# Optimization experiments

Hardware: AMD Instinct MI355X
Metric: run time of the kernel (lower is better)

Reference implementation:

```python
import jax, jax.numpy as jnp
import numpy as np

F4_MAX = 6.0      # float4 e2m1 max magnitude
F8_MAX = 448.0    # float8 e4m3 max magnitude
BLOCK = 16        # nvfp4 block size along reduction dim


def _fp4_e2m1_rne(v):
    """Round v to the nearest float4 e2m1 value, ties-to-even.
    Representable magnitudes: {0, 0.5, 1, 1.5, 2, 3, 4, 6}."""
    s = jnp.sign(v)
    a = jnp.clip(jnp.abs(v), 0.0, F4_MAX)
    # exponent of the quantization step: subnormals and [1,2) share step 0.5
    e = jnp.clip(jnp.floor(jnp.log2(jnp.maximum(a, 1.0))), 0.0, 2.0)
    step = jnp.exp2(e - 1.0)  # 0.5, 1.0 or 2.0
    q = jnp.round(a / step) * step  # jnp.round is round-half-to-even
    return s * jnp.clip(q, 0.0, F4_MAX)


def _nvfp4_quant_dequant(x, global_scale):
    """scaled_fp4_quant followed by dequant (== what the scaled fp4 GEMM
    with alpha = 1/(gs_a*gs_w) computes per operand)."""
    lead, K = x.shape[:-1], x.shape[-1]
    xb = x.reshape(*lead, K // BLOCK, BLOCK)
    amax = jnp.max(jnp.abs(xb), axis=-1, keepdims=True)            # per-block amax
    scale = (amax * (global_scale / F4_MAX))
    scale = scale.astype(jnp.float8_e4m3fn).astype(jnp.float32)    # e4m3 block scale
    safe = jnp.where(scale > 0.0, scale, 1.0)
    q = _fp4_e2m1_rne(xb * (global_scale / safe))                  # fp4 codes (as floats)
    dq = q * safe / global_scale                                   # dequantized values
    return dq.reshape(x.shape)


def setup_inputs() -> dict:
    key = jax.random.key(0)
    k1, k2, k3 = jax.random.split(key, 3)
    B, S, K, N = 4, 2048, 4096, 4096
    x = jax.random.normal(k1, (B, S, K), dtype=jnp.float32)
    W = jax.random.normal(k2, (N, K), dtype=jnp.float32) * 0.02
    bias = jax.random.normal(k3, (N,), dtype=jnp.float32) * 0.02
    return {"x": x, "W": W, "bias": bias}


def reference(x, W, bias):
    # per-tensor global scales (FLOAT8_E4M3_MAX * FLOAT4_E2M1_MAX / amax)
    x_gs = (F8_MAX * F4_MAX) / jnp.max(jnp.abs(x)).astype(jnp.float32)
    w_gs = (F8_MAX * F4_MAX) / jnp.max(jnp.abs(W)).astype(jnp.float32)
    x_dq = _nvfp4_quant_dequant(x, x_gs)   # [B,S,K]
    w_dq = _nvfp4_quant_dequant(W, w_gs)   # [N,K]
    out = jnp.einsum('bsk,nk->bsn', x_dq, w_dq) + bias
    return out.astype(x.dtype)
```

## Files before the change

kernel.cpp:

```cpp
#include <hip/hip_runtime.h>
#include <stdint.h>

typedef unsigned short u16;
typedef __bf16 bf16x8 __attribute__((ext_vector_type(8)));
typedef float floatx4 __attribute__((ext_vector_type(4)));

__global__ void amax_both_k(const float4* __restrict__ x, long nx4,
                            const float4* __restrict__ w, long nw4,
                            unsigned* slots, int gx) {
    const float4* src; long n4; int bid, nb; unsigned* slot;
    if ((int)blockIdx.x < gx) { src = x; n4 = nx4; bid = blockIdx.x; nb = gx; slot = slots; }
    else { src = w; n4 = nw4; bid = blockIdx.x - gx; nb = gridDim.x - gx; slot = slots + 1; }
    float m = 0.0f;
    long stride = (long)nb * blockDim.x;
    for (long i = (long)bid * blockDim.x + threadIdx.x; i < n4; i += stride) {
        float4 v = src[i];
        m = fmaxf(m, fmaxf(fmaxf(fabsf(v.x), fabsf(v.y)), fmaxf(fabsf(v.z), fabsf(v.w))));
    }
    #pragma unroll
    for (int off = 32; off > 0; off >>= 1)
        m = fmaxf(m, __shfl_down(m, off, 64));
    __shared__ float sm[4];
    int lane = threadIdx.x & 63, wv = threadIdx.x >> 6;
    if (lane == 0) sm[wv] = m;
    __syncthreads();
    if (threadIdx.x == 0) {
        m = fmaxf(fmaxf(sm[0], sm[1]), fmaxf(sm[2], sm[3]));
        atomicMax(slot, __float_as_uint(m));
    }
}

__device__ __forceinline__ float e4m3_rne(float v) {
    unsigned u = __float_as_uint(v);
    u += 0x7FFFFu + ((u >> 20) & 1u);
    float hi = __uint_as_float(u & 0xFFF00000u);
    float lo = rintf(v * 512.0f) * 0.001953125f;
    return (v < 0.015625f) ? lo : hi;
}

__device__ __forceinline__ float fp4_rne(float x) {
    float a = fminf(fabsf(x), 6.0f);
    unsigned u = __float_as_uint(a);
    u += 0x1FFFFFu + ((u >> 22) & 1u);
    float hi = __uint_as_float(u & 0xFFC00000u);
    float lo = rintf(a + a) * 0.5f;
    float q = (a < 1.0f) ? lo : hi;
    return copysignf(q, x);
}

__device__ __forceinline__ unsigned pack2(float d0, float d1) {
    return (__float_as_uint(d0) >> 16) | (__float_as_uint(d1) & 0xFFFF0000u);
}

__global__ void quant_both_k(const float* __restrict__ x, const float* __restrict__ W,
                             u16* __restrict__ Aq, u16* __restrict__ Bq,
                             const unsigned* __restrict__ slots, long nbx, long nbtot) {
    long b = (long)blockIdx.x * blockDim.x + threadIdx.x;
    if (b >= nbtot) return;
    const float* src; u16* dst; float ag;
    if (b < nbx) { src = x + b * 16; dst = Aq + b * 16; ag = __uint_as_float(slots[0]); }
    else { long c = b - nbx; src = W + c * 16; dst = Bq + c * 16; ag = __uint_as_float(slots[1]); }
    float gs = 2688.0f / ag;
    float t  = gs / 6.0f;
    const float4* p = (const float4*)src;
    float4 v0 = p[0], v1 = p[1], v2 = p[2], v3 = p[3];
    float am = 0.0f;
    am = fmaxf(am, fmaxf(fmaxf(fabsf(v0.x), fabsf(v0.y)), fmaxf(fabsf(v0.z), fabsf(v0.w))));
    am = fmaxf(am, fmaxf(fmaxf(fabsf(v1.x), fabsf(v1.y)), fmaxf(fabsf(v1.z), fabsf(v1.w))));
    am = fmaxf(am, fmaxf(fmaxf(fabsf(v2.x), fabsf(v2.y)), fmaxf(fabsf(v2.z), fabsf(v2.w))));
    am = fmaxf(am, fmaxf(fmaxf(fabsf(v3.x), fabsf(v3.y)), fmaxf(fabsf(v3.z), fabsf(v3.w))));
    float sf = e4m3_rne(am * t);
    float r = gs / (sf > 0.0f ? sf : 1.0f);
    uint4 o0, o1;
    o0.x = pack2(fp4_rne(v0.x * r) * sf, fp4_rne(v0.y * r) * sf);
    o0.y = pack2(fp4_rne(v0.z * r) * sf, fp4_rne(v0.w * r) * sf);
    o0.z = pack2(fp4_rne(v1.x * r) * sf, fp4_rne(v1.y * r) * sf);
    o0.w = pack2(fp4_rne(v1.z * r) * sf, fp4_rne(v1.w * r) * sf);
    o1.x = pack2(fp4_rne(v2.x * r) * sf, fp4_rne(v2.y * r) * sf);
    o1.y = pack2(fp4_rne(v2.z * r) * sf, fp4_rne(v2.w * r) * sf);
    o1.z = pack2(fp4_rne(v3.x * r) * sf, fp4_rne(v3.y * r) * sf);
    o1.w = pack2(fp4_rne(v3.z * r) * sf, fp4_rne(v3.w * r) * sf);
    uint4* q = (uint4*)dst;
    q[0] = o0; q[1] = o1;
}

#define KTILE 64

#define SFENCE() __builtin_amdgcn_sched_barrier(0)
#define BAR() do { asm volatile("" ::: "memory"); SFENCE(); \
    __builtin_amdgcn_s_barrier(); SFENCE(); asm volatile("" ::: "memory"); } while (0)

#define STAGE_SLOT(GS, LS) do { \
    __builtin_amdgcn_global_load_lds((const __attribute__((address_space(1))) void*)(GS), \
        (__attribute__((address_space(3))) void*)(LS), 16, 0, 0); \
    __builtin_amdgcn_global_load_lds((const __attribute__((address_space(1))) void*)((GS) + row64K), \
        (__attribute__((address_space(3))) void*)((LS) + 4096), 16, 0, 0); \
} while (0)

#define LDA(CUR, MH) do { \
    _Pragma("unroll") for (int mf = 0; mf < 4; ++mf) { \
        const u16* p_ = aB + (CUR) * 16384 + ((MH) * 64 + mf * 16) * 64; \
        af[mf][0] = *(const bf16x8*)(p_ + ca0 * 8); \
        af[mf][1] = *(const bf16x8*)(p_ + ca1 * 8); \
    } } while (0)

#define LDB(CUR, NH) do { \
    _Pragma("unroll") for (int nf = 0; nf < 2; ++nf) { \
        const u16* p_ = bB + (CUR) * 16384 + ((NH) * 32 + nf * 16) * 64; \
        bf[(NH)*2+nf][0] = *(const bf16x8*)(p_ + ca0 * 8); \
        bf[(NH)*2+nf][1] = *(const bf16x8*)(p_ + ca1 * 8); \
    } } while (0)

#define QUAD(MH, NH) do { \
    _Pragma("unroll") for (int ks = 0; ks < 2; ++ks) \
    _Pragma("unroll") for (int mf = 0; mf < 4; ++mf) \
    _Pragma("unroll") for (int nf = 0; nf < 2; ++nf) \
        acc[(MH)*4+mf][(NH)*2+nf] = __builtin_amdgcn_mfma_f32_16x16x32_bf16( \
            af[mf][ks], bf[(NH)*2+nf][ks], acc[(MH)*4+mf][(NH)*2+nf], 0, 0, 0); \
} while (0)

#define TILE(CUR, S) do { \
    const u16* gA1 = Ag + (size_t)(((S)+1 < NT) ? (S)+1 : NT-1) * KTILE; \
    const u16* gB2 = Bg + (size_t)(((S)+2 < NT) ? (S)+2 : NT-1) * KTILE; \
    u16* lA1 = Al + ((CUR)^1) * 16384; \
    u16* lB2 = Bl + (CUR) * 16384; \
     \
    LDA(CUR, 0); LDB(CUR, 0); \
    STAGE_SLOT(gA1, lA1); \
    BAR(); \
    __builtin_amdgcn_s_setprio(1); QUAD(0, 0); __builtin_amdgcn_s_setprio(0); \
    BAR(); \
     \
    LDB(CUR, 1); \
    STAGE_SLOT(gA1 + halfGA, lA1 + 8192); \
    BAR(); \
    __builtin_amdgcn_s_setprio(1); QUAD(0, 1); __builtin_amdgcn_s_setprio(0); \
    BAR(); \
     \
    LDA(CUR, 1); \
    STAGE_SLOT(gB2, lB2); \
    BAR(); \
    __builtin_amdgcn_s_setprio(1); QUAD(1, 0); __builtin_amdgcn_s_setprio(0); \
    BAR(); \
     \
    STAGE_SLOT(gB2 + halfGA, lB2 + 8192); \
    BAR(); \
    __builtin_amdgcn_s_setprio(1); QUAD(1, 1); __builtin_amdgcn_s_setprio(0); \
    SFENCE(); \
    asm volatile("s_waitcnt vmcnt(4)" ::: "memory"); \
    BAR(); \
} while (0)

__global__ __launch_bounds__(512, 2) void gemm_k(
    const u16* __restrict__ A, const u16* __restrict__ B,
    const float* __restrict__ bias, const unsigned* __restrict__ scal,
    float* __restrict__ out, int M, int N, int K)
{
    __shared__ u16 As[2 * 256 * 64];
    __shared__ u16 Bs[2 * 256 * 64];

    const int tid = threadIdx.x;
    const int l   = tid & 63;
    const int wv  = tid >> 6;
    const int wm  = wv >> 2;
    const int wn  = wv & 3;

    const int nTM = M / 256, nTN = N / 256;
    const int nwg = nTM * nTN;
    const int orig = blockIdx.x;
    const int xcd = orig & 7, lid = orig >> 3;
    const int q8 = nwg >> 3, r8 = nwg & 7;
    const int swz = (xcd < r8 ? xcd * (q8 + 1) : r8 * (q8 + 1) + (xcd - r8) * q8) + lid;
    const long tileM = (long)(swz % nTM) * 256;
    const long tileN = (long)(swz / nTM) * 256;

    const int srow  = tid >> 3;
    const int sslot = tid & 7;
    const int schunk = sslot ^ (srow & 7);
    const size_t row64K = (size_t)64 * K;
    const size_t halfGA = (size_t)128 * K;
    const u16* Ag = A + (size_t)(tileM + srow) * K + schunk * 8;
    const u16* Bg = B + (size_t)(tileN + srow) * K + schunk * 8;
    u16* Al = As + wv * 512;
    u16* Bl = Bs + wv * 512;

    const int lr = l & 15;
    const int hi = l >> 4;
    const int ca0 = hi ^ (lr & 7);
    const int ca1 = ca0 ^ 4;
    const u16* aB = As + (wm * 128 + lr) * 64;
    const u16* bB = Bs + (wn * 64 + lr) * 64;

    floatx4 acc[8][4] = {};
    bf16x8 af[4][2], bf[4][2];

    const int NT = K / KTILE;

    STAGE_SLOT(Bg, Bl);
    STAGE_SLOT(Bg + halfGA, Bl + 8192);
    STAGE_SLOT(Ag, Al);
    STAGE_SLOT(Ag + halfGA, Al + 8192);
    {
        const u16* gB1 = Bg + ((1 < NT) ? KTILE : 0);
        STAGE_SLOT(gB1, Bl + 16384);
        STAGE_SLOT(gB1 + halfGA, Bl + 16384 + 8192);
    }
    SFENCE();
    asm volatile("s_waitcnt vmcnt(4)" ::: "memory");
    BAR();

    for (int s = 0; s < NT; s += 2) {
        TILE(0, s);
        TILE(1, s + 1);
    }

    float ax = __uint_as_float(scal[0]);
    float aw = __uint_as_float(scal[1]);
    float gsx = 2688.0f / ax, gsw = 2688.0f / aw;
    float alpha = 1.0f / (gsx * gsw);

    #pragma unroll
    for (int nq = 0; nq < 4; ++nq) {
        const long col = tileN + wn * 64 + nq * 16 + lr;
        const float bv = bias[col];
        #pragma unroll
        for (int mq = 0; mq < 8; ++mq) {
            const long r0 = tileM + wm * 128 + mq * 16 + hi * 4;
            #pragma unroll
            for (int reg = 0; reg < 4; ++reg)
                out[(size_t)(r0 + reg) * N + col] = acc[mq][nq][reg] * alpha + bv;
        }
    }
}

extern "C" void kernel_launch(void* const* d_in, const int* in_sizes, int n_in,
                              void* d_out, int out_size, void* d_ws, size_t ws_size,
                              hipStream_t stream) {
    const float* x    = (const float*)d_in[0];
    const float* W    = (const float*)d_in[1];
    const float* bias = (const float*)d_in[2];
    float* out = (float*)d_out;

    const int N = in_sizes[2];
    const int K = in_sizes[1] / N;
    const int M = in_sizes[0] / K;

    unsigned* scal = (unsigned*)d_ws;
    u16* Aq = (u16*)((char*)d_ws + 256);
    u16* Bq = Aq + (size_t)M * K;

    hipMemsetAsync(scal, 0, 8, stream);

    const int GX = 2048, GW = 1024;
    hipLaunchKernelGGL(amax_both_k, dim3(GX + GW), dim3(256), 0, stream,
                       (const float4*)x, (long)M * K / 4,
                       (const float4*)W, (long)N * K / 4, scal, GX);

    long nbx = (long)M * K / 16;
    long nbw = (long)N * K / 16;
    hipLaunchKernelGGL(quant_both_k, dim3((unsigned)((nbx + nbw + 255) / 256)), dim3(256), 0, stream,
                       x, W, Aq, Bq, scal, nbx, nbx + nbw);

    hipLaunchKernelGGL(gemm_k, dim3((M / 256) * (N / 256)), dim3(512), 0, stream,
                       Aq, Bq, bias, scal, out, M, N, K);
}
```

Baseline: 581.2 us.

## Double-buffer LDS fragment reads in GEMM and coalesce quant kernel via lane shuffles

```diff
diff --git a/kernel.cpp b/kernel.cpp
--- a/kernel.cpp
+++ b/kernel.cpp
@@ -52,36 +52,29 @@
     return (__float_as_uint(d0) >> 16) | (__float_as_uint(d1) & 0xFFFF0000u);
 }
 
-__global__ void quant_both_k(const float* __restrict__ x, const float* __restrict__ W,
-                             u16* __restrict__ Aq, u16* __restrict__ Bq,
-                             const unsigned* __restrict__ slots, long nbx, long nbtot) {
-    long b = (long)blockIdx.x * blockDim.x + threadIdx.x;
-    if (b >= nbtot) return;
-    const float* src; u16* dst; float ag;
-    if (b < nbx) { src = x + b * 16; dst = Aq + b * 16; ag = __uint_as_float(slots[0]); }
-    else { long c = b - nbx; src = W + c * 16; dst = Bq + c * 16; ag = __uint_as_float(slots[1]); }
-    float gs = 2688.0f / ag;
-    float t  = gs / 6.0f;
-    const float4* p = (const float4*)src;
-    float4 v0 = p[0], v1 = p[1], v2 = p[2], v3 = p[3];
-    float am = 0.0f;
-    am = fmaxf(am, fmaxf(fmaxf(fabsf(v0.x), fabsf(v0.y)), fmaxf(fabsf(v0.z), fabsf(v0.w))));
-    am = fmaxf(am, fmaxf(fmaxf(fabsf(v1.x), fabsf(v1.y)), fmaxf(fabsf(v1.z), fabsf(v1.w))));
-    am = fmaxf(am, fmaxf(fmaxf(fabsf(v2.x), fabsf(v2.y)), fmaxf(fabsf(v2.z), fabsf(v2.w))));
-    am = fmaxf(am, fmaxf(fmaxf(fabsf(v3.x), fabsf(v3.y)), fmaxf(fabsf(v3.z), fabsf(v3.w))));
-    float sf = e4m3_rne(am * t);
-    float r = gs / (sf > 0.0f ? sf : 1.0f);
-    uint4 o0, o1;
-    o0.x = pack2(fp4_rne(v0.x * r) * sf, fp4_rne(v0.y * r) * sf);
-    o0.y = pack2(fp4_rne(v0.z * r) * sf, fp4_rne(v0.w * r) * sf);
-    o0.z = pack2(fp4_rne(v1.x * r) * sf, fp4_rne(v1.y * r) * sf);
-    o0.w = pack2(fp4_rne(v1.z * r) * sf, fp4_rne(v1.w * r) * sf);
-    o1.x = pack2(fp4_rne(v2.x * r) * sf, fp4_rne(v2.y * r) * sf);
-    o1.y = pack2(fp4_rne(v2.z * r) * sf, fp4_rne(v2.w * r) * sf);
-    o1.z = pack2(fp4_rne(v3.x * r) * sf, fp4_rne(v3.y * r) * sf);
-    o1.w = pack2(fp4_rne(v3.z * r) * sf, fp4_rne(v3.w * r) * sf);
-    uint4* q = (uint4*)dst;
-    q[0] = o0; q[1] = o1;
+__global__ void quant_both_k(const float4* __restrict__ x4, const float4* __restrict__ w4,
+                             uint2* __restrict__ Aq2, uint2* __restrict__ Bq2,
+                             const unsigned* __restrict__ slots, long nx4, long ntot4) {
+    float ag0 = __uint_as_float(slots[0]);
+    float ag1 = __uint_as_float(slots[1]);
+    float gs0 = 2688.0f / ag0, gs1 = 2688.0f / ag1;
+    float t0 = gs0 / 6.0f,     t1 = gs1 / 6.0f;
+    long stride = (long)gridDim.x * blockDim.x;
+    for (long i = (long)blockIdx.x * blockDim.x + threadIdx.x; i < ntot4; i += stride) {
+        bool isx = i < nx4;
+        float4 v = isx ? x4[i] : w4[i - nx4];
+        float gs = isx ? gs0 : gs1;
+        float t  = isx ? t0  : t1;
+        float am = fmaxf(fmaxf(fabsf(v.x), fabsf(v.y)), fmaxf(fabsf(v.z), fabsf(v.w)));
+        am = fmaxf(am, __shfl_xor(am, 1, 4));
+        am = fmaxf(am, __shfl_xor(am, 2, 4));
+        float sf = e4m3_rne(am * t);
+        float r = gs / (sf > 0.0f ? sf : 1.0f);
+        uint2 o;
+        o.x = pack2(fp4_rne(v.x * r) * sf, fp4_rne(v.y * r) * sf);
+        o.y = pack2(fp4_rne(v.z * r) * sf, fp4_rne(v.w * r) * sf);
+        if (isx) Aq2[i] = o; else Bq2[i - nx4] = o;
+    }
 }
 
 #define KTILE 64
@@ -89,6 +82,9 @@
 #define SFENCE() __builtin_amdgcn_sched_barrier(0)
 #define BAR() do { asm volatile("" ::: "memory"); SFENCE(); \
     __builtin_amdgcn_s_barrier(); SFENCE(); asm volatile("" ::: "memory"); } while (0)
+
+#define DSR128O(D, VB, IMM) asm volatile("ds_read_b128 %0, %1 offset:%c2" \
+    : "=v"(D) : "v"(VB), "i"(IMM))
 
 #define STAGE_SLOT(GS, LS) do { \
     __builtin_amdgcn_global_load_lds((const __attribute__((address_space(1))) void*)(GS), \
@@ -97,57 +93,67 @@
         (__attribute__((address_space(3))) void*)((LS) + 4096), 16, 0, 0); \
 } while (0)
 
-#define LDA(CUR, MH) do { \
-    _Pragma("unroll") for (int mf = 0; mf < 4; ++mf) { \
-        const u16* p_ = aB + (CUR) * 16384 + ((MH) * 64 + mf * 16) * 64; \
-        af[mf][0] = *(const bf16x8*)(p_ + ca0 * 8); \
-        af[mf][1] = *(const bf16x8*)(p_ + ca1 * 8); \
-    } } while (0)
-
-#define LDB(CUR, NH) do { \
-    _Pragma("unroll") for (int nf = 0; nf < 2; ++nf) { \
-        const u16* p_ = bB + (CUR) * 16384 + ((NH) * 32 + nf * 16) * 64; \
-        bf[(NH)*2+nf][0] = *(const bf16x8*)(p_ + ca0 * 8); \
-        bf[(NH)*2+nf][1] = *(const bf16x8*)(p_ + ca1 * 8); \
-    } } while (0)
-
-#define QUAD(MH, NH) do { \
+#define LDA_TO(SET, CURLIT, MH) do { \
+    DSR128O(SET[0][0], vA0, ((CURLIT)*32768+(((MH)*64+ 0)*128))); \
+    DSR128O(SET[0][1], vA1, ((CURLIT)*32768+(((MH)*64+ 0)*128))); \
+    DSR128O(SET[1][0], vA0, ((CURLIT)*32768+(((MH)*64+16)*128))); \
+    DSR128O(SET[1][1], vA1, ((CURLIT)*32768+(((MH)*64+16)*128))); \
+    DSR128O(SET[2][0], vA0, ((CURLIT)*32768+(((MH)*64+32)*128))); \
+    DSR128O(SET[2][1], vA1, ((CURLIT)*32768+(((MH)*64+32)*128))); \
+    DSR128O(SET[3][0], vA0, ((CURLIT)*32768+(((MH)*64+48)*128))); \
+    DSR128O(SET[3][1], vA1, ((CURLIT)*32768+(((MH)*64+48)*128))); \
+} while (0)
+
+#define LDB_TO(SET, CURLIT, NH) do { \
+    DSR128O(SET[0][0], vB0, ((CURLIT)*32768+(((NH)*32+ 0)*128))); \
+    DSR128O(SET[0][1], vB1, ((CURLIT)*32768+(((NH)*32+ 0)*128))); \
+    DSR128O(SET[1][0], vB0, ((CURLIT)*32768+(((NH)*32+16)*128))); \
+    DSR128O(SET[1][1], vB1, ((CURLIT)*32768+(((NH)*32+16)*128))); \
+} while (0)
+
+#define QUADS(AS, BS, MH, NH) do { \
     _Pragma("unroll") for (int ks = 0; ks < 2; ++ks) \
     _Pragma("unroll") for (int mf = 0; mf < 4; ++mf) \
     _Pragma("unroll") for (int nf = 0; nf < 2; ++nf) \
         acc[(MH)*4+mf][(NH)*2+nf] = __builtin_amdgcn_mfma_f32_16x16x32_bf16( \
-            af[mf][ks], bf[(NH)*2+nf][ks], acc[(MH)*4+mf][(NH)*2+nf], 0, 0, 0); \
-} while (0)
-
-#define TILE(CUR, S) do { \
+            AS[mf][ks], BS[nf][ks], acc[(MH)*4+mf][(NH)*2+nf], 0, 0, 0); \
+} while (0)
+
+#define TILE(CUR, NXT, S) do { \
     const u16* gA1 = Ag + (size_t)(((S)+1 < NT) ? (S)+1 : NT-1) * KTILE; \
+    const u16* gA2 = Ag + (size_t)(((S)+2 < NT) ? (S)+2 : NT-1) * KTILE; \
     const u16* gB2 = Bg + (size_t)(((S)+2 < NT) ? (S)+2 : NT-1) * KTILE; \
-    u16* lA1 = Al + ((CUR)^1) * 16384; \
+    u16* lA1 = Al + (NXT) * 16384; \
+    u16* lA2 = Al + (CUR) * 16384; \
     u16* lB2 = Bl + (CUR) * 16384; \
      \
-    LDA(CUR, 0); LDB(CUR, 0); \
-    STAGE_SLOT(gA1, lA1); \
-    BAR(); \
-    __builtin_amdgcn_s_setprio(1); QUAD(0, 0); __builtin_amdgcn_s_setprio(0); \
-    BAR(); \
-     \
-    LDB(CUR, 1); \
+    LDB_TO(bf_b, CUR, 1); \
     STAGE_SLOT(gA1 + halfGA, lA1 + 8192); \
     BAR(); \
-    __builtin_amdgcn_s_setprio(1); QUAD(0, 1); __builtin_amdgcn_s_setprio(0); \
-    BAR(); \
-     \
-    LDA(CUR, 1); \
+    asm volatile("s_waitcnt lgkmcnt(4)" ::: "memory"); SFENCE(); \
+    __builtin_amdgcn_s_setprio(1); QUADS(af_a, bf_a, 0, 0); __builtin_amdgcn_s_setprio(0); \
+    BAR(); \
+     \
+    LDA_TO(af_b, CUR, 1); \
+    BAR(); \
+    asm volatile("s_waitcnt lgkmcnt(8)" ::: "memory"); SFENCE(); \
+    __builtin_amdgcn_s_setprio(1); QUADS(af_a, bf_b, 0, 1); __builtin_amdgcn_s_setprio(0); \
+    BAR(); \
+     \
     STAGE_SLOT(gB2, lB2); \
     BAR(); \
-    __builtin_amdgcn_s_setprio(1); QUAD(1, 0); __builtin_amdgcn_s_setprio(0); \
-    BAR(); \
-     \
+    asm volatile("s_waitcnt lgkmcnt(0)" ::: "memory"); SFENCE(); \
+    __builtin_amdgcn_s_setprio(1); QUADS(af_b, bf_a, 1, 0); __builtin_amdgcn_s_setprio(0); \
+    SFENCE(); \
+    asm volatile("s_waitcnt vmcnt(2)" ::: "memory"); \
+    BAR(); \
+     \
+    LDA_TO(af_a, NXT, 0); \
+    LDB_TO(bf_a, NXT, 0); \
     STAGE_SLOT(gB2 + halfGA, lB2 + 8192); \
-    BAR(); \
-    __builtin_amdgcn_s_setprio(1); QUAD(1, 1); __builtin_amdgcn_s_setprio(0); \
-    SFENCE(); \
-    asm volatile("s_waitcnt vmcnt(4)" ::: "memory"); \
+    STAGE_SLOT(gA2, lA2); \
+    BAR(); \
+    __builtin_amdgcn_s_setprio(1); QUADS(af_b, bf_b, 1, 1); __builtin_amdgcn_s_setprio(0); \
     BAR(); \
 } while (0)
 
@@ -188,11 +194,17 @@
     const int hi = l >> 4;
     const int ca0 = hi ^ (lr & 7);
     const int ca1 = ca0 ^ 4;
-    const u16* aB = As + (wm * 128 + lr) * 64;
-    const u16* bB = Bs + (wn * 64 + lr) * 64;
+    const unsigned vA0 = (unsigned)(unsigned long long)
+        (const __attribute__((address_space(3))) void*)(const void*)(As + (wm * 128 + lr) * 64 + ca0 * 8);
+    const unsigned vA1 = (unsigned)(unsigned long long)
+        (const __attribute__((address_space(3))) void*)(const void*)(As + (wm * 128 + lr) * 64 + ca1 * 8);
+    const unsigned vB0 = (unsigned)(unsigned long long)
+        (const __attribute__((address_space(3))) void*)(const void*)(Bs + (wn * 64 + lr) * 64 + ca0 * 8);
+    const unsigned vB1 = (unsigned)(unsigned long long)
+        (const __attribute__((address_space(3))) void*)(const void*)(Bs + (wn * 64 + lr) * 64 + ca1 * 8);
 
     floatx4 acc[8][4] = {};
-    bf16x8 af[4][2], bf[4][2];
+    bf16x8 af_a[4][2], af_b[4][2], bf_a[2][2], bf_b[2][2];
 
     const int NT = K / KTILE;
 
@@ -201,18 +213,26 @@
     STAGE_SLOT(Ag, Al);
     STAGE_SLOT(Ag + halfGA, Al + 8192);
     {
-        const u16* gB1 = Bg + ((1 < NT) ? KTILE : 0);
+        const u16* gB1 = Bg + (size_t)((1 < NT) ? 1 : 0) * KTILE;
         STAGE_SLOT(gB1, Bl + 16384);
         STAGE_SLOT(gB1 + halfGA, Bl + 16384 + 8192);
+        const u16* gA1p = Ag + (size_t)((1 < NT) ? 1 : 0) * KTILE;
+        STAGE_SLOT(gA1p, Al + 16384);
     }
     SFENCE();
-    asm volatile("s_waitcnt vmcnt(4)" ::: "memory");
+    asm volatile("s_waitcnt vmcnt(6)" ::: "memory");
     BAR();
+    LDA_TO(af_a, 0, 0);
+    LDB_TO(bf_a, 0, 0);
 
     for (int s = 0; s < NT; s += 2) {
-        TILE(0, s);
-        TILE(1, s + 1);
-    }
+        TILE(0, 1, s);
+        TILE(1, 0, s + 1);
+    }
+
+    SFENCE();
+    asm volatile("s_waitcnt vmcnt(0) lgkmcnt(0)" ::: "memory");
+    SFENCE();
 
     float ax = __uint_as_float(scal[0]);
     float aw = __uint_as_float(scal[1]);
@@ -256,10 +276,11 @@
                        (const float4*)x, (long)M * K / 4,
                        (const float4*)W, (long)N * K / 4, scal, GX);
 
-    long nbx = (long)M * K / 16;
-    long nbw = (long)N * K / 16;
-    hipLaunchKernelGGL(quant_both_k, dim3((unsigned)((nbx + nbw + 255) / 256)), dim3(256), 0, stream,
-                       x, W, Aq, Bq, scal, nbx, nbx + nbw);
+    long nx4 = (long)M * K / 4;
+    long nw4 = (long)N * K / 4;
+    hipLaunchKernelGGL(quant_both_k, dim3(4096), dim3(256), 0, stream,
+                       (const float4*)x, (const float4*)W,
+                       (uint2*)Aq, (uint2*)Bq, scal, nx4, nx4 + nw4);
 
     hipLaunchKernelGGL(gemm_k, dim3((M / 256) * (N / 256)), dim3(512), 0, stream,
                        Aq, Bq, bias, scal, out, M, N, K);
```

Result: faster. 538.1 us (-7.4%).
